# Kernel tuning notes

Measured on AMD Instinct MI355X. Metric: run time of the kernel, lower is better.

## Reference

```python
import jax, jax.numpy as jnp
import numpy as np

HIDDEN = 2048
HEADS = 16
HEAD_DIM = HIDDEN // HEADS  # 128


def setup_inputs() -> dict:
    key = jax.random.key(0)
    ks = jax.random.split(key, 9)
    B, S = 2, 2048
    x = jax.random.normal(ks[0], (B, S, HIDDEN), dtype=jnp.float32)
    scale = 1.0 / np.sqrt(HIDDEN)
    Wq = jax.random.normal(ks[1], (HIDDEN, HIDDEN), dtype=jnp.float32) * scale
    Wk = jax.random.normal(ks[2], (HIDDEN, HIDDEN), dtype=jnp.float32) * scale
    Wv = jax.random.normal(ks[3], (HIDDEN, HIDDEN), dtype=jnp.float32) * scale
    Wo = jax.random.normal(ks[4], (HIDDEN, HIDDEN), dtype=jnp.float32) * scale
    bq = jnp.zeros((HIDDEN,), dtype=jnp.float32)
    bk = jnp.zeros((HIDDEN,), dtype=jnp.float32)
    bv = jnp.zeros((HIDDEN,), dtype=jnp.float32)
    bo = jnp.zeros((HIDDEN,), dtype=jnp.float32)
    return {"x": x, "Wq": Wq, "bq": bq, "Wk": Wk, "bk": bk,
            "Wv": Wv, "bv": bv, "Wo": Wo, "bo": bo}


def reference(x, Wq, bq, Wk, bk, Wv, bv, Wo, bo):
    B, S, H = x.shape
    nh, hd = HEADS, HEAD_DIM
    # projections: Linear stores W as [out, in], applies x @ W.T + b
    q = (x @ Wq.T + bq).reshape(B, S, nh, hd).transpose(0, 2, 1, 3)  # [B,nh,S,hd]
    k = (x @ Wk.T + bk).reshape(B, S, nh, hd).transpose(0, 2, 1, 3)
    v = (x @ Wv.T + bv).reshape(B, S, nh, hd).transpose(0, 2, 1, 3)
    scores = jnp.einsum("bhqd,bhkd->bhqk", q, k) / np.sqrt(hd)  # [B,nh,S,S]
    causal = jnp.tril(jnp.ones((S, S), dtype=bool))
    scores = jnp.where(causal[None, None], scores, -jnp.inf)
    probs = jax.nn.softmax(scores, axis=-1)
    attn = jnp.einsum("bhqk,bhkd->bhqd", probs, v)  # [B,nh,S,hd]
    y = attn.transpose(0, 2, 1, 3).reshape(B, S, H)
    return y @ Wo.T + bo
```

## Files before the change

### kernel.cpp

```cpp
#include <hip/hip_runtime.h>

#define HIDDEN 2048
#define NH 16
#define HD 128
#define BATCH 2
#define SEQ 2048

typedef __attribute__((ext_vector_type(8))) short short8;
typedef __attribute__((ext_vector_type(4))) float floatx4;

__device__ inline unsigned short f2bf(float f) {
  union { float f; unsigned int u; } x; x.f = f;
  unsigned int r = x.u + 0x7fffu + ((x.u >> 16) & 1u);
  return (unsigned short)(r >> 16);
}
__device__ inline unsigned int pkbf(float a, float b) {
  return (unsigned int)f2bf(a) | ((unsigned int)f2bf(b) << 16);
}

__device__ inline void async_cp16(const void* g, void* l) {
  __builtin_amdgcn_global_load_lds(
      (const __attribute__((address_space(1))) unsigned int*)g,
      (__attribute__((address_space(3))) unsigned int*)l, 16, 0, 0);
}

__global__ __launch_bounds__(256) void cvt_kernel(const float* __restrict__ in,
                                                  unsigned short* __restrict__ out,
                                                  int n) {
  int i = (blockIdx.x * 256 + threadIdx.x) * 4;
  if (i + 3 < n) {
    float4 v = *reinterpret_cast<const float4*>(in + i);
    ushort4 o;
    o.x = f2bf(v.x); o.y = f2bf(v.y); o.z = f2bf(v.z); o.w = f2bf(v.w);
    *reinterpret_cast<ushort4*>(out + i) = o;
  }
}

template<int MODE>
__global__ __launch_bounds__(256) void gemm_nt(const unsigned short* __restrict__ A,
                                               const unsigned short* __restrict__ Bw,
                                               const float* __restrict__ bias,
                                               float* __restrict__ outF,
                                               unsigned short* __restrict__ outQ) {
  __shared__ __align__(16) unsigned short As[2][4096];
  __shared__ __align__(16) unsigned short Bs[2][4096];
  const int t = threadIdx.x;
  const int lane = t & 63;
  const int w = t >> 6;
  const int wr = w >> 1, wc = w & 1;
  const int row0 = blockIdx.x * 128;
  const int col0 = blockIdx.y * 128;

  floatx4 acc[4][4] = {};

#pragma unroll
  for (int cc = 0; cc < 2; ++cc) {
    int c = t + cc * 256;
    int k8 = c >> 7, r = c & 127;
    async_cp16(A + (size_t)(row0 + r) * 2048 + k8 * 8, &As[0][c * 8]);
    async_cp16(Bw + (size_t)(col0 + r) * 2048 + k8 * 8, &Bs[0][c * 8]);
  }
  __syncthreads();

  int buf = 0;
  for (int kt = 0; kt < 64; ++kt) {
    if (kt < 63) {
      const int kb = (kt + 1) * 32;
#pragma unroll
      for (int cc = 0; cc < 2; ++cc) {
        int c = t + cc * 256;
        int k8 = c >> 7, r = c & 127;
        async_cp16(A + (size_t)(row0 + r) * 2048 + kb + k8 * 8, &As[buf ^ 1][c * 8]);
        async_cp16(Bw + (size_t)(col0 + r) * 2048 + kb + k8 * 8, &Bs[buf ^ 1][c * 8]);
      }
    }
    short8 af[4], bf[4];
#pragma unroll
    for (int m = 0; m < 4; ++m)
      af[m] = *(const short8*)&As[buf][(lane >> 4) * 1024 + (wr * 64 + m * 16 + (lane & 15)) * 8];
#pragma unroll
    for (int n = 0; n < 4; ++n)
      bf[n] = *(const short8*)&Bs[buf][(lane >> 4) * 1024 + (wc * 64 + n * 16 + (lane & 15)) * 8];
#pragma unroll
    for (int m = 0; m < 4; ++m)
#pragma unroll
      for (int n = 0; n < 4; ++n)
        acc[m][n] = __builtin_amdgcn_mfma_f32_16x16x32_bf16(af[m], bf[n], acc[m][n], 0, 0, 0);
    __syncthreads();
    buf ^= 1;
  }

#pragma unroll
  for (int m = 0; m < 4; ++m) {
#pragma unroll
    for (int n = 0; n < 4; ++n) {
      int gcol = col0 + wc * 64 + n * 16 + (lane & 15);
      float bv = bias[gcol];
#pragma unroll
      for (int r = 0; r < 4; ++r) {
        int grow = row0 + wr * 64 + m * 16 + (lane >> 4) * 4 + r;
        float v = acc[m][n][r] + bv;
        if (MODE == 1) {
          outF[(size_t)grow * 2048 + gcol] = v;
        } else {
          int bb = grow >> 11;
          int ss = grow & 2047;
          int hh = gcol >> 7;
          int dd = gcol & 127;
          outQ[(((size_t)bb * NH + hh) * SEQ + ss) * HD + dd] = f2bf(v);
        }
      }
    }
  }
}

__global__ __launch_bounds__(256) void attn_kernel(const unsigned short* __restrict__ Q,
                                                   const unsigned short* __restrict__ Kg,
                                                   const unsigned short* __restrict__ Vg,
                                                   unsigned short* __restrict__ O) {
  __shared__ __align__(16) unsigned short Ks[16 * 64 * 8];
  __shared__ __align__(16) unsigned short VT[8 * 128 * 8];

  const int t = threadIdx.x;
  const int lane = t & 63;
  const int w = t >> 6;
  const int g = lane >> 4;
  const int l15 = lane & 15;

  int gid = blockIdx.x;
  int Wi = (gid < 256) ? gid : 767 - gid;
  const int bx = Wi & 15;
  const int bh = Wi >> 4;
  const int q0 = bx * 128;
  const int bb = bh >> 4;
  const int hh = bh & 15;

  const unsigned short* Qb = Q + (size_t)bh * SEQ * HD;
  const unsigned short* Kb = Kg + (size_t)bh * SEQ * HD;
  const unsigned short* Vb = Vg + (size_t)bh * SEQ * HD;

  const int qw = q0 + w * 32;

  short8 bq[2][4];
#pragma unroll
  for (int qh = 0; qh < 2; ++qh)
#pragma unroll
    for (int kb = 0; kb < 4; ++kb)
      bq[qh][kb] = *(const short8*)(Qb + (size_t)(qw + qh * 16 + l15) * HD + kb * 32 + g * 8);

  floatx4 acc[2][8] = {};
  float mrun[2] = {-1e30f, -1e30f};
  float lrun[2] = {0.f, 0.f};
  const float scale = 0.08838834764831845f;

  const int ntiles = (q0 >> 6) + 2;
  for (int tk = 0; tk < ntiles; ++tk) {
    const int k0 = tk * 64;
    __syncthreads();
#pragma unroll
    for (int cc = 0; cc < 4; ++cc) {
      int c = t + cc * 256;
      int k8 = c >> 6, s = c & 63;
      int kvs = ((s >> 5) << 5) + (((s >> 2) & 3) << 3) + (((s >> 4) & 1) << 2) + (s & 3);
      async_cp16(Kb + (size_t)(k0 + kvs) * HD + k8 * 8, &Ks[c * 8]);
    }
#pragma unroll
    for (int cc = 0; cc < 2; ++cc) {
      int c = t + cc * 256;
      int kv = (c >> 4) * 2;
      int d0 = (c & 15) * 8;
      int row = kv >> 3;
      short8 va = *(const short8*)(Vb + (size_t)(k0 + kv) * HD + d0);
      short8 vb = *(const short8*)(Vb + (size_t)(k0 + kv + 1) * HD + d0);
#pragma unroll
      for (int j = 0; j < 8; ++j) {
        int d = d0 + j;
        int dp = d ^ (((d >> 3) ^ row) & 7);
        unsigned int u = (unsigned short)va[j] | ((unsigned int)(unsigned short)vb[j] << 16);
        *(unsigned int*)&VT[(row * 128 + dp) * 8 + (kv & 7)] = u;
      }
    }
    __syncthreads();

    floatx4 sv[4][2];
#pragma unroll
    for (int kvh = 0; kvh < 4; ++kvh) {
      sv[kvh][0] = (floatx4){0.f, 0.f, 0.f, 0.f};
      sv[kvh][1] = (floatx4){0.f, 0.f, 0.f, 0.f};
#pragma unroll
      for (int kb = 0; kb < 4; ++kb) {
        short8 ak = *(const short8*)&Ks[((kb * 4 + g) * 64 + kvh * 16 + l15) * 8];
        sv[kvh][0] = __builtin_amdgcn_mfma_f32_16x16x32_bf16(ak, bq[0][kb], sv[kvh][0], 0, 0, 0);
        sv[kvh][1] = __builtin_amdgcn_mfma_f32_16x16x32_bf16(ak, bq[1][kb], sv[kvh][1], 0, 0, 0);
      }
    }

    const bool domask = (k0 + 63 > qw);
#pragma unroll
    for (int kvh = 0; kvh < 4; ++kvh)
#pragma unroll
      for (int qh = 0; qh < 2; ++qh)
#pragma unroll
        for (int r = 0; r < 4; ++r) {
          float s = sv[kvh][qh][r] * scale;
          if (domask) {
            int kvg = k0 + ((kvh >> 1) << 5) + g * 8 + ((kvh & 1) << 2) + r;
            int qg = qw + qh * 16 + l15;
            if (kvg > qg) s = -1e30f;
          }
          sv[kvh][qh][r] = s;
        }

#pragma unroll
    for (int qh = 0; qh < 2; ++qh) {
      float mt = sv[0][qh][0];
#pragma unroll
      for (int kvh = 0; kvh < 4; ++kvh)
#pragma unroll
        for (int r = 0; r < 4; ++r)
          mt = fmaxf(mt, sv[kvh][qh][r]);
      mt = fmaxf(mt, __shfl_xor(mt, 16, 64));
      mt = fmaxf(mt, __shfl_xor(mt, 32, 64));
      float mnew = fmaxf(mrun[qh], mt);
      float f = __expf(mrun[qh] - mnew);
      mrun[qh] = mnew;
      float ssum = 0.f;
#pragma unroll
      for (int kvh = 0; kvh < 4; ++kvh)
#pragma unroll
        for (int r = 0; r < 4; ++r) {
          float p = __expf(sv[kvh][qh][r] - mnew);
          sv[kvh][qh][r] = p;
          ssum += p;
        }
      ssum += __shfl_xor(ssum, 16, 64);
      ssum += __shfl_xor(ssum, 32, 64);
      lrun[qh] = lrun[qh] * f + ssum;
      float fr[4];
#pragma unroll
      for (int r = 0; r < 4; ++r)
        fr[r] = __shfl(f, (lane & 48) + 4 * (lane >> 4) + r, 64);
#pragma unroll
      for (int db = 0; db < 8; ++db)
#pragma unroll
        for (int r = 0; r < 4; ++r)
          acc[qh][db][r] *= fr[r];
    }

#pragma unroll
    for (int kh = 0; kh < 2; ++kh) {
      union { short8 s8; unsigned int u[4]; } p0, p1;
      p0.u[0] = pkbf(sv[2 * kh][0][0], sv[2 * kh][0][1]);
      p0.u[1] = pkbf(sv[2 * kh][0][2], sv[2 * kh][0][3]);
      p0.u[2] = pkbf(sv[2 * kh + 1][0][0], sv[2 * kh + 1][0][1]);
      p0.u[3] = pkbf(sv[2 * kh + 1][0][2], sv[2 * kh + 1][0][3]);
      p1.u[0] = pkbf(sv[2 * kh][1][0], sv[2 * kh][1][1]);
      p1.u[1] = pkbf(sv[2 * kh][1][2], sv[2 * kh][1][3]);
      p1.u[2] = pkbf(sv[2 * kh + 1][1][0], sv[2 * kh + 1][1][1]);
      p1.u[3] = pkbf(sv[2 * kh + 1][1][2], sv[2 * kh + 1][1][3]);
      int row = kh * 4 + g;
#pragma unroll
      for (int db = 0; db < 8; ++db) {
        int d = db * 16 + l15;
        int dp = d ^ (((d >> 3) ^ row) & 7);
        short8 bv = *(const short8*)&VT[(row * 128 + dp) * 8];
        acc[0][db] = __builtin_amdgcn_mfma_f32_16x16x32_bf16(p0.s8, bv, acc[0][db], 0, 0, 0);
        acc[1][db] = __builtin_amdgcn_mfma_f32_16x16x32_bf16(p1.s8, bv, acc[1][db], 0, 0, 0);
      }
    }
  }

#pragma unroll
  for (int qh = 0; qh < 2; ++qh) {
    float inv = 1.0f / lrun[qh];
    float ir[4];
#pragma unroll
    for (int r = 0; r < 4; ++r)
      ir[r] = __shfl(inv, (lane & 48) + 4 * (lane >> 4) + r, 64);
#pragma unroll
    for (int r = 0; r < 4; ++r) {
      int qg = qw + qh * 16 + 4 * g + r;
      size_t base = ((size_t)bb * SEQ + qg) * HIDDEN + hh * HD;
#pragma unroll
      for (int db = 0; db < 8; ++db)
        O[base + db * 16 + l15] = f2bf(acc[qh][db][r] * ir[r]);
    }
  }
}

extern "C" void kernel_launch(void* const* d_in, const int* in_sizes, int n_in,
                              void* d_out, int out_size, void* d_ws, size_t ws_size,
                              hipStream_t stream) {
  (void)in_sizes; (void)n_in; (void)out_size; (void)ws_size;
  const float* x  = (const float*)d_in[0];
  const float* Wq = (const float*)d_in[1];
  const float* bq = (const float*)d_in[2];
  const float* Wk = (const float*)d_in[3];
  const float* bk = (const float*)d_in[4];
  const float* Wv = (const float*)d_in[5];
  const float* bv = (const float*)d_in[6];
  const float* Wo = (const float*)d_in[7];
  const float* bo = (const float*)d_in[8];
  float* out = (float*)d_out;

  char* ws = (char*)d_ws;
  unsigned short* xbf = (unsigned short*)ws;
  unsigned short* Wbf = (unsigned short*)(ws + 16777216);
  unsigned short* Qbf = (unsigned short*)(ws + 25165824);
  unsigned short* Kbf = (unsigned short*)(ws + 41943040);
  unsigned short* Vbf = (unsigned short*)(ws + 58720256);

  dim3 blk(256);
  dim3 gg(32, 16);
  dim3 ga(512);

  cvt_kernel<<<8192, blk, 0, stream>>>(x, xbf, BATCH * SEQ * HIDDEN);

  cvt_kernel<<<4096, blk, 0, stream>>>(Wq, Wbf, HIDDEN * HIDDEN);
  gemm_nt<0><<<gg, blk, 0, stream>>>(xbf, Wbf, bq, nullptr, Qbf);

  cvt_kernel<<<4096, blk, 0, stream>>>(Wk, Wbf, HIDDEN * HIDDEN);
  gemm_nt<0><<<gg, blk, 0, stream>>>(xbf, Wbf, bk, nullptr, Kbf);

  cvt_kernel<<<4096, blk, 0, stream>>>(Wv, Wbf, HIDDEN * HIDDEN);
  gemm_nt<0><<<gg, blk, 0, stream>>>(xbf, Wbf, bv, nullptr, Vbf);

  attn_kernel<<<ga, blk, 0, stream>>>(Qbf, Kbf, Vbf, xbf);

  cvt_kernel<<<4096, blk, 0, stream>>>(Wo, Wbf, HIDDEN * HIDDEN);
  gemm_nt<1><<<gg, blk, 0, stream>>>(xbf, Wbf, bo, out, nullptr);
}
```

Measured before the change: 615.1 us.

## Fuse QKV GEMMs, double-buffer attention K/V, and add lazy softmax rescaling

```diff
diff --git a/kernel.cpp b/kernel.cpp
--- a/kernel.cpp
+++ b/kernel.cpp
@@ -36,20 +36,35 @@
   }
 }
 
+struct QkvPtrs {
+  const unsigned short* W[3];
+  const float* b[3];
+  unsigned short* oq[3];
+  float oscale[3];
+};
+
 template<int MODE>
-__global__ __launch_bounds__(256) void gemm_nt(const unsigned short* __restrict__ A,
-                                               const unsigned short* __restrict__ Bw,
-                                               const float* __restrict__ bias,
-                                               float* __restrict__ outF,
-                                               unsigned short* __restrict__ outQ) {
+__global__ __launch_bounds__(256, 4) void gemm_nt(const unsigned short* __restrict__ A,
+                                                  QkvPtrs P,
+                                                  float* __restrict__ outF) {
   __shared__ __align__(16) unsigned short As[2][4096];
   __shared__ __align__(16) unsigned short Bs[2][4096];
   const int t = threadIdx.x;
   const int lane = t & 63;
   const int w = t >> 6;
   const int wr = w >> 1, wc = w & 1;
-  const int row0 = blockIdx.x * 128;
-  const int col0 = blockIdx.y * 128;
+
+  const int nwg = gridDim.x;
+  int bid = blockIdx.x;
+  int Wi = (bid & 7) * (nwg >> 3) + (bid >> 3);
+  const int bx = Wi & 31;
+  const int by = Wi >> 5;
+  const int wsel = (MODE == 0) ? (by >> 4) : 0;
+  const int row0 = bx * 128;
+  const int col0 = (by & 15) * 128;
+
+  const unsigned short* Bw = P.W[wsel];
+  const float* bias = P.b[wsel];
 
   floatx4 acc[4][4] = {};
 
@@ -90,6 +105,7 @@
     buf ^= 1;
   }
 
+  const float osc = P.oscale[wsel];
 #pragma unroll
   for (int m = 0; m < 4; ++m) {
 #pragma unroll
@@ -107,7 +123,7 @@
           int ss = grow & 2047;
           int hh = gcol >> 7;
           int dd = gcol & 127;
-          outQ[(((size_t)bb * NH + hh) * SEQ + ss) * HD + dd] = f2bf(v);
+          P.oq[wsel][(((size_t)bb * NH + hh) * SEQ + ss) * HD + dd] = f2bf(v * osc);
         }
       }
     }
@@ -118,8 +134,8 @@
                                                    const unsigned short* __restrict__ Kg,
                                                    const unsigned short* __restrict__ Vg,
                                                    unsigned short* __restrict__ O) {
-  __shared__ __align__(16) unsigned short Ks[16 * 64 * 8];
-  __shared__ __align__(16) unsigned short VT[8 * 128 * 8];
+  __shared__ __align__(16) unsigned short Ks[2][16 * 64 * 8];
+  __shared__ __align__(16) unsigned short VT[2][8 * 128 * 8];
 
   const int t = threadIdx.x;
   const int lane = t & 63;
@@ -151,36 +167,62 @@
   floatx4 acc[2][8] = {};
   float mrun[2] = {-1e30f, -1e30f};
   float lrun[2] = {0.f, 0.f};
-  const float scale = 0.08838834764831845f;
+
+  short8 vreg[4];
+  const int vkv = (t >> 4) * 2;
+  const int vd0 = (t & 15) * 8;
 
   const int ntiles = (q0 >> 6) + 2;
-  for (int tk = 0; tk < ntiles; ++tk) {
-    const int k0 = tk * 64;
-    __syncthreads();
+
+  {
 #pragma unroll
     for (int cc = 0; cc < 4; ++cc) {
       int c = t + cc * 256;
       int k8 = c >> 6, s = c & 63;
       int kvs = ((s >> 5) << 5) + (((s >> 2) & 3) << 3) + (((s >> 4) & 1) << 2) + (s & 3);
-      async_cp16(Kb + (size_t)(k0 + kvs) * HD + k8 * 8, &Ks[c * 8]);
+      async_cp16(Kb + (size_t)kvs * HD + k8 * 8, &Ks[0][c * 8]);
     }
 #pragma unroll
     for (int cc = 0; cc < 2; ++cc) {
-      int c = t + cc * 256;
-      int kv = (c >> 4) * 2;
-      int d0 = (c & 15) * 8;
+      vreg[cc * 2]     = *(const short8*)(Vb + (size_t)(vkv + cc * 32) * HD + vd0);
+      vreg[cc * 2 + 1] = *(const short8*)(Vb + (size_t)(vkv + cc * 32 + 1) * HD + vd0);
+    }
+#pragma unroll
+    for (int cc = 0; cc < 2; ++cc) {
+      int kv = vkv + cc * 32;
       int row = kv >> 3;
-      short8 va = *(const short8*)(Vb + (size_t)(k0 + kv) * HD + d0);
-      short8 vb = *(const short8*)(Vb + (size_t)(k0 + kv + 1) * HD + d0);
 #pragma unroll
       for (int j = 0; j < 8; ++j) {
-        int d = d0 + j;
+        int d = vd0 + j;
         int dp = d ^ (((d >> 3) ^ row) & 7);
-        unsigned int u = (unsigned short)va[j] | ((unsigned int)(unsigned short)vb[j] << 16);
-        *(unsigned int*)&VT[(row * 128 + dp) * 8 + (kv & 7)] = u;
+        unsigned int u = (unsigned short)vreg[cc * 2][j] |
+                         ((unsigned int)(unsigned short)vreg[cc * 2 + 1][j] << 16);
+        *(unsigned int*)&VT[0][(row * 128 + dp) * 8 + (kv & 7)] = u;
       }
     }
     __syncthreads();
+  }
+
+  for (int tk = 0; tk < ntiles; ++tk) {
+    const int buf = tk & 1;
+    const int k0 = tk * 64;
+    const bool pf = (tk + 1 < ntiles);
+
+    if (pf) {
+      const int kn = k0 + 64;
+#pragma unroll
+      for (int cc = 0; cc < 4; ++cc) {
+        int c = t + cc * 256;
+        int k8 = c >> 6, s = c & 63;
+        int kvs = ((s >> 5) << 5) + (((s >> 2) & 3) << 3) + (((s >> 4) & 1) << 2) + (s & 3);
+        async_cp16(Kb + (size_t)(kn + kvs) * HD + k8 * 8, &Ks[buf ^ 1][c * 8]);
+      }
+#pragma unroll
+      for (int cc = 0; cc < 2; ++cc) {
+        vreg[cc * 2]     = *(const short8*)(Vb + (size_t)(kn + vkv + cc * 32) * HD + vd0);
+        vreg[cc * 2 + 1] = *(const short8*)(Vb + (size_t)(kn + vkv + cc * 32 + 1) * HD + vd0);
+      }
+    }
 
     floatx4 sv[4][2];
 #pragma unroll
@@ -189,27 +231,24 @@
       sv[kvh][1] = (floatx4){0.f, 0.f, 0.f, 0.f};
 #pragma unroll
       for (int kb = 0; kb < 4; ++kb) {
-        short8 ak = *(const short8*)&Ks[((kb * 4 + g) * 64 + kvh * 16 + l15) * 8];
+        short8 ak = *(const short8*)&Ks[buf][((kb * 4 + g) * 64 + kvh * 16 + l15) * 8];
         sv[kvh][0] = __builtin_amdgcn_mfma_f32_16x16x32_bf16(ak, bq[0][kb], sv[kvh][0], 0, 0, 0);
         sv[kvh][1] = __builtin_amdgcn_mfma_f32_16x16x32_bf16(ak, bq[1][kb], sv[kvh][1], 0, 0, 0);
       }
     }
 
-    const bool domask = (k0 + 63 > qw);
-#pragma unroll
-    for (int kvh = 0; kvh < 4; ++kvh)
-#pragma unroll
-      for (int qh = 0; qh < 2; ++qh)
-#pragma unroll
-        for (int r = 0; r < 4; ++r) {
-          float s = sv[kvh][qh][r] * scale;
-          if (domask) {
+    if (k0 + 63 > qw) {
+#pragma unroll
+      for (int kvh = 0; kvh < 4; ++kvh)
+#pragma unroll
+        for (int qh = 0; qh < 2; ++qh)
+#pragma unroll
+          for (int r = 0; r < 4; ++r) {
             int kvg = k0 + ((kvh >> 1) << 5) + g * 8 + ((kvh & 1) << 2) + r;
             int qg = qw + qh * 16 + l15;
-            if (kvg > qg) s = -1e30f;
+            if (kvg > qg) sv[kvh][qh][r] = -1e30f;
           }
-          sv[kvh][qh][r] = s;
-        }
+    }
 
 #pragma unroll
     for (int qh = 0; qh < 2; ++qh) {
@@ -221,30 +260,34 @@
           mt = fmaxf(mt, sv[kvh][qh][r]);
       mt = fmaxf(mt, __shfl_xor(mt, 16, 64));
       mt = fmaxf(mt, __shfl_xor(mt, 32, 64));
-      float mnew = fmaxf(mrun[qh], mt);
-      float f = __expf(mrun[qh] - mnew);
-      mrun[qh] = mnew;
+      if (__any(mt > mrun[qh] + 8.0f)) {
+        float mnew = fmaxf(mrun[qh], mt);
+        float f = __expf(mrun[qh] - mnew);
+        mrun[qh] = mnew;
+        lrun[qh] *= f;
+        float fr[4];
+#pragma unroll
+        for (int r = 0; r < 4; ++r)
+          fr[r] = __shfl(f, (lane & 48) + 4 * g + r, 64);
+#pragma unroll
+        for (int db = 0; db < 8; ++db)
+#pragma unroll
+          for (int r = 0; r < 4; ++r)
+            acc[qh][db][r] *= fr[r];
+      }
+      float m = mrun[qh];
       float ssum = 0.f;
 #pragma unroll
       for (int kvh = 0; kvh < 4; ++kvh)
 #pragma unroll
         for (int r = 0; r < 4; ++r) {
-          float p = __expf(sv[kvh][qh][r] - mnew);
+          float p = __expf(sv[kvh][qh][r] - m);
           sv[kvh][qh][r] = p;
           ssum += p;
         }
       ssum += __shfl_xor(ssum, 16, 64);
       ssum += __shfl_xor(ssum, 32, 64);
-      lrun[qh] = lrun[qh] * f + ssum;
-      float fr[4];
-#pragma unroll
-      for (int r = 0; r < 4; ++r)
-        fr[r] = __shfl(f, (lane & 48) + 4 * (lane >> 4) + r, 64);
-#pragma unroll
-      for (int db = 0; db < 8; ++db)
-#pragma unroll
-        for (int r = 0; r < 4; ++r)
-          acc[qh][db][r] *= fr[r];
+      lrun[qh] += ssum;
     }
 
 #pragma unroll
@@ -263,10 +306,27 @@
       for (int db = 0; db < 8; ++db) {
         int d = db * 16 + l15;
         int dp = d ^ (((d >> 3) ^ row) & 7);
-        short8 bv = *(const short8*)&VT[(row * 128 + dp) * 8];
+        short8 bv = *(const short8*)&VT[buf][(row * 128 + dp) * 8];
         acc[0][db] = __builtin_amdgcn_mfma_f32_16x16x32_bf16(p0.s8, bv, acc[0][db], 0, 0, 0);
         acc[1][db] = __builtin_amdgcn_mfma_f32_16x16x32_bf16(p1.s8, bv, acc[1][db], 0, 0, 0);
       }
+    }
+
+    if (pf) {
+#pragma unroll
+      for (int cc = 0; cc < 2; ++cc) {
+        int kv = vkv + cc * 32;
+        int row = kv >> 3;
+#pragma unroll
+        for (int j = 0; j < 8; ++j) {
+          int d = vd0 + j;
+          int dp = d ^ (((d >> 3) ^ row) & 7);
+          unsigned int u = (unsigned short)vreg[cc * 2][j] |
+                           ((unsigned int)(unsigned short)vreg[cc * 2 + 1][j] << 16);
+          *(unsigned int*)&VT[buf ^ 1][(row * 128 + dp) * 8 + (kv & 7)] = u;
+        }
+      }
+      __syncthreads();
     }
   }
 
@@ -276,7 +336,7 @@
     float ir[4];
 #pragma unroll
     for (int r = 0; r < 4; ++r)
-      ir[r] = __shfl(inv, (lane & 48) + 4 * (lane >> 4) + r, 64);
+      ir[r] = __shfl(inv, (lane & 48) + 4 * g + r, 64);
 #pragma unroll
     for (int r = 0; r < 4; ++r) {
       int qg = qw + qh * 16 + 4 * g + r;
@@ -291,7 +351,7 @@
 extern "C" void kernel_launch(void* const* d_in, const int* in_sizes, int n_in,
                               void* d_out, int out_size, void* d_ws, size_t ws_size,
                               hipStream_t stream) {
-  (void)in_sizes; (void)n_in; (void)out_size; (void)ws_size;
+  (void)in_sizes; (void)n_in; (void)out_size;
   const float* x  = (const float*)d_in[0];
   const float* Wq = (const float*)d_in[1];
   const float* bq = (const float*)d_in[2];
@@ -303,30 +363,72 @@
   const float* bo = (const float*)d_in[8];
   float* out = (float*)d_out;
 
+  const float qscale = 0.08838834764831845f;
   char* ws = (char*)d_ws;
-  unsigned short* xbf = (unsigned short*)ws;
-  unsigned short* Wbf = (unsigned short*)(ws + 16777216);
-  unsigned short* Qbf = (unsigned short*)(ws + 25165824);
-  unsigned short* Kbf = (unsigned short*)(ws + 41943040);
-  unsigned short* Vbf = (unsigned short*)(ws + 58720256);
-
   dim3 blk(256);
-  dim3 gg(32, 16);
-  dim3 ga(512);
-
-  cvt_kernel<<<8192, blk, 0, stream>>>(x, xbf, BATCH * SEQ * HIDDEN);
-
-  cvt_kernel<<<4096, blk, 0, stream>>>(Wq, Wbf, HIDDEN * HIDDEN);
-  gemm_nt<0><<<gg, blk, 0, stream>>>(xbf, Wbf, bq, nullptr, Qbf);
-
-  cvt_kernel<<<4096, blk, 0, stream>>>(Wk, Wbf, HIDDEN * HIDDEN);
-  gemm_nt<0><<<gg, blk, 0, stream>>>(xbf, Wbf, bk, nullptr, Kbf);
-
-  cvt_kernel<<<4096, blk, 0, stream>>>(Wv, Wbf, HIDDEN * HIDDEN);
-  gemm_nt<0><<<gg, blk, 0, stream>>>(xbf, Wbf, bv, nullptr, Vbf);
-
-  attn_kernel<<<ga, blk, 0, stream>>>(Qbf, Kbf, Vbf, xbf);
-
-  cvt_kernel<<<4096, blk, 0, stream>>>(Wo, Wbf, HIDDEN * HIDDEN);
-  gemm_nt<1><<<gg, blk, 0, stream>>>(xbf, Wbf, bo, out, nullptr);
-}
+  const bool fused = ws_size >= 92274688ull;
+
+  if (fused) {
+    unsigned short* xbf = (unsigned short*)ws;
+    unsigned short* W0  = (unsigned short*)(ws + 16777216);
+    unsigned short* W1  = (unsigned short*)(ws + 25165824);
+    unsigned short* W2  = (unsigned short*)(ws + 33554432);
+    unsigned short* Qbf = (unsigned short*)(ws + 41943040);
+    unsigned short* Kbf = (unsigned short*)(ws + 58720256);
+    unsigned short* Vbf = (unsigned short*)(ws + 75497472);
+
+    cvt_kernel<<<8192, blk, 0, stream>>>(x, xbf, BATCH * SEQ * HIDDEN);
+    cvt_kernel<<<4096, blk, 0, stream>>>(Wq, W0, HIDDEN * HIDDEN);
+    cvt_kernel<<<4096, blk, 0, stream>>>(Wk, W1, HIDDEN * HIDDEN);
+    cvt_kernel<<<4096, blk, 0, stream>>>(Wv, W2, HIDDEN * HIDDEN);
+
+    QkvPtrs Pq;
+    Pq.W[0] = W0;  Pq.W[1] = W1;  Pq.W[2] = W2;
+    Pq.b[0] = bq;  Pq.b[1] = bk;  Pq.b[2] = bv;
+    Pq.oq[0] = Qbf; Pq.oq[1] = Kbf; Pq.oq[2] = Vbf;
+    Pq.oscale[0] = qscale; Pq.oscale[1] = 1.0f; Pq.oscale[2] = 1.0f;
+    gemm_nt<0><<<1536, blk, 0, stream>>>(xbf, Pq, nullptr);
+
+    attn_kernel<<<512, blk, 0, stream>>>(Qbf, Kbf, Vbf, xbf);
+
+    cvt_kernel<<<4096, blk, 0, stream>>>(Wo, W0, HIDDEN * HIDDEN);
+    QkvPtrs Po;
+    Po.W[0] = W0; Po.W[1] = W0; Po.W[2] = W0;
+    Po.b[0] = bo; Po.b[1] = bo; Po.b[2] = bo;
+    Po.oq[0] = nullptr; Po.oq[1] = nullptr; Po.oq[2] = nullptr;
+    Po.oscale[0] = 1.0f; Po.oscale[1] = 1.0f; Po.oscale[2] = 1.0f;
+    gemm_nt<1><<<512, blk, 0, stream>>>(xbf, Po, out);
+  } else {
+    unsigned short* xbf = (unsigned short*)ws;
+    unsigned short* Wbf = (unsigned short*)(ws + 16777216);
+    unsigned short* Qbf = (unsigned short*)(ws + 25165824);
+    unsigned short* Kbf = (unsigned short*)(ws + 41943040);
+    unsigned short* Vbf = (unsigned short*)(ws + 58720256);
+
+    cvt_kernel<<<8192, blk, 0, stream>>>(x, xbf, BATCH * SEQ * HIDDEN);
+
+    const float* biases[3] = {bq, bk, bv};
+    const float* wsrc[3] = {Wq, Wk, Wv};
+    unsigned short* outs[3] = {Qbf, Kbf, Vbf};
+    float oscales[3] = {qscale, 1.0f, 1.0f};
+    for (int i = 0; i < 3; ++i) {
+      cvt_kernel<<<4096, blk, 0, stream>>>(wsrc[i], Wbf, HIDDEN * HIDDEN);
+      QkvPtrs Pp;
+      Pp.W[0] = Wbf; Pp.W[1] = Wbf; Pp.W[2] = Wbf;
+      Pp.b[0] = biases[i]; Pp.b[1] = biases[i]; Pp.b[2] = biases[i];
+      Pp.oq[0] = outs[i]; Pp.oq[1] = outs[i]; Pp.oq[2] = outs[i];
+      Pp.oscale[0] = oscales[i]; Pp.oscale[1] = oscales[i]; Pp.oscale[2] = oscales[i];
+      gemm_nt<0><<<512, blk, 0, stream>>>(xbf, Pp, nullptr);
+    }
+
+    attn_kernel<<<512, blk, 0, stream>>>(Qbf, Kbf, Vbf, xbf);
+
+    cvt_kernel<<<4096, blk, 0, stream>>>(Wo, Wbf, HIDDEN * HIDDEN);
+    QkvPtrs Po;
+    Po.W[0] = Wbf; Po.W[1] = Wbf; Po.W[2] = Wbf;
+    Po.b[0] = bo; Po.b[1] = bo; Po.b[2] = bo;
+    Po.oq[0] = nullptr; Po.oq[1] = nullptr; Po.oq[2] = nullptr;
+    Po.oscale[0] = 1.0f; Po.oscale[1] = 1.0f; Po.oscale[2] = 1.0f;
+    gemm_nt<1><<<512, blk, 0, stream>>>(xbf, Po, out);
+  }
+}
```

Result: faster. 600.9 us (-2.3%).
